# Performance work log

Hardware: AMD Instinct MI355X
Metric: run time of the kernel (lower is better)

The kernel has to match this reference:

```python
import jax, jax.numpy as jnp
import numpy as np

B, S, E = 4, 2048, 1024

def setup_inputs() -> dict:
    key = jax.random.key(0)
    ks = jax.random.split(key, 4)
    scale = 1.0 / np.sqrt(E)
    x = jax.random.normal(ks[0], (B, S, E), dtype=jnp.float32)
    Wq = jax.random.normal(ks[1], (E, E), dtype=jnp.float32) * scale
    Wk = jax.random.normal(ks[2], (E, E), dtype=jnp.float32) * scale
    Wv = jax.random.normal(ks[3], (E, E), dtype=jnp.float32) * scale
    bq = jnp.zeros((E,), dtype=jnp.float32)
    bk = jnp.zeros((E,), dtype=jnp.float32)
    bv = jnp.zeros((E,), dtype=jnp.float32)
    # causal mask: 1 where attention allowed, 0 where blocked (masked_fill(mask==0, -inf))
    mask = jnp.tril(jnp.ones((S, S), dtype=jnp.int32))
    return {"x": x, "mask": mask, "Wq": Wq, "bq": bq, "Wk": Wk, "bk": bk, "Wv": Wv, "bv": bv}

def reference(x, mask, Wq, bq, Wk, bk, Wv, bv):
    # x: (B, S, E); mask: (S, S) int, 0 -> -inf. Matches torch nn.Linear: x @ W.T + b
    Q = jnp.einsum('bse,fe->bsf', x, Wq) + bq
    K = jnp.einsum('bse,fe->bsf', x, Wk) + bk
    V = jnp.einsum('bse,fe->bsf', x, Wv) + bv
    inv_sqrt_e = 1.0 / jnp.sqrt(jnp.asarray(x.shape[-1], dtype=x.dtype))
    scores = jnp.einsum('bqe,bke->bqk', Q, K) * inv_sqrt_e  # (B, S, S)
    scores = jnp.where(mask[None, :, :] == 0, jnp.asarray(-jnp.inf, scores.dtype), scores)
    attn = jax.nn.softmax(scores, axis=-1)
    out = jnp.einsum('bqk,bke->bqe', attn, V)  # (B, S, E)
    return out
```

## Files before the change

kernel.cpp:

```cpp
#include <hip/hip_runtime.h>

#define B_ 4
#define S_ 2048
#define E_ 1024

typedef __attribute__((ext_vector_type(8))) short short8;
typedef __attribute__((ext_vector_type(4))) float f32x4;

__device__ __forceinline__ unsigned short f2bu(float f) {
  unsigned u = __builtin_bit_cast(unsigned, f);
  u = (u + 0x7FFFu + ((u >> 16) & 1u)) >> 16;
  return (unsigned short)u;
}

__device__ __forceinline__ void gload_lds16(const void* g, void* l) {
  __builtin_amdgcn_global_load_lds(
      (const __attribute__((address_space(1))) void*)g,
      (__attribute__((address_space(3))) void*)l, 16, 0, 0);
}

__global__ __launch_bounds__(256) void cvt_f32_bf16(
    const float* __restrict__ in, unsigned short* __restrict__ out, int n) {
  int i = blockIdx.x * 256 + threadIdx.x;
  if (i * 4 >= n) return;
  float4 v = ((const float4*)in)[i];
  ushort4 o;
  o.x = f2bu(v.x); o.y = f2bu(v.y); o.z = f2bu(v.z); o.w = f2bu(v.w);
  ((ushort4*)out)[i] = o;
}

__global__ __launch_bounds__(256) void cvt_w3(
    const float* __restrict__ w0, const float* __restrict__ w1,
    const float* __restrict__ w2, unsigned short* __restrict__ out, int n) {
  int z = blockIdx.z;
  const float* in = (z == 0) ? w0 : (z == 1) ? w1 : w2;
  int i = blockIdx.x * 256 + threadIdx.x;
  if (i * 4 >= n) return;
  float4 v = ((const float4*)in)[i];
  ushort4 o;
  o.x = f2bu(v.x); o.y = f2bu(v.y); o.z = f2bu(v.z); o.w = f2bu(v.w);
  ((ushort4*)(out + (long)z * n))[i] = o;
}

__global__ __launch_bounds__(256) void zden(float* __restrict__ d) {
  ((float4*)d)[blockIdx.x * 256 + threadIdx.x] = float4{0.f, 0.f, 0.f, 0.f};
}

template<int MODE>
__device__ __forceinline__ void gemm_body(
    const unsigned short* __restrict__ A, long sAz, int lda,
    const unsigned short* __restrict__ B, long sBz, int ldb,
    const float* __restrict__ bias0, const float* __restrict__ bias1,
    const float* __restrict__ bias2,
    void* __restrict__ C0, void* __restrict__ C1, void* __restrict__ C2,
    long sCz, int ldc, int K, float scale, float* __restrict__ denom,
    unsigned short* lA, unsigned short* lB, int bm, int bn, int bz) {
  constexpr int BK = 64;
  const unsigned short* Ab = A + (long)bz * sAz + (long)bm * 128 * lda;
  const unsigned short* Bb = B + (long)bz * sBz + (long)bn * 128 * ldb;
  int Keff = (MODE == 2) ? min(K, (bm + 1) * 128) : K;

  int tid = threadIdx.x;
  int l = tid & 63, w = tid >> 6;
  int wm = w >> 1, wn = w & 1;

  int srow = l >> 3;
  int schunk = (l & 7) * 8;
  const unsigned short* ga[4];
  const unsigned short* gb[4];
  unsigned short* lad[4];
  unsigned short* lbd[4];
#pragma unroll
  for (int i = 0; i < 4; i++) {
    int seg = i * 4 + w;
    int row = seg * 8 + srow;
    ga[i] = Ab + (long)row * lda + schunk;
    gb[i] = Bb + (long)row * ldb + schunk;
    lad[i] = &lA[seg * 512];
    lbd[i] = &lB[seg * 512];
  }
  int aoff[4], boff[4];
#pragma unroll
  for (int i = 0; i < 4; i++) {
    aoff[i] = (wm * 64 + i * 16 + (l & 15)) * BK + (l >> 4) * 8;
    boff[i] = (wn * 64 + i * 16 + (l & 15)) * BK + (l >> 4) * 8;
  }

  f32x4 acc[4][4] = {};

  for (int k0 = 0; k0 < Keff; k0 += BK) {
    __syncthreads();
#pragma unroll
    for (int i = 0; i < 4; i++) {
      gload_lds16(ga[i], lad[i]);
      gload_lds16(gb[i], lbd[i]);
    }
#pragma unroll
    for (int i = 0; i < 4; i++) { ga[i] += BK; gb[i] += BK; }
    __syncthreads();
#pragma unroll
    for (int kk = 0; kk < 2; kk++) {
      short8 af[4], bf[4];
#pragma unroll
      for (int i = 0; i < 4; i++) af[i] = *(const short8*)&lA[aoff[i] + kk * 32];
#pragma unroll
      for (int j = 0; j < 4; j++) bf[j] = *(const short8*)&lB[boff[j] + kk * 32];
#pragma unroll
      for (int i = 0; i < 4; i++)
#pragma unroll
        for (int j = 0; j < 4; j++)
          acc[i][j] = __builtin_amdgcn_mfma_f32_16x16x32_bf16(af[i], bf[j], acc[i][j], 0, 0, 0);
    }
  }

  int rh = l >> 4, cl = l & 15;
  long rowbase = (long)bm * 128 + wm * 64 + rh * 4;
  int colbase = bn * 128 + wn * 64 + cl;

  if constexpr (MODE == 0) {
    int seg = bn >> 3;
    const float* bias = (seg == 0) ? bias0 : (seg == 1) ? bias1 : bias2;
#pragma unroll
    for (int j = 0; j < 4; j++) {
      int c = colbase + j * 16;
      int cl_ = c & 1023;
      float bv_ = bias[cl_];
#pragma unroll
      for (int i = 0; i < 4; i++) {
        long r0 = rowbase + i * 16;
        f32x4 v = acc[i][j];
        if (seg < 2) {
          unsigned short* Ch = (unsigned short*)((seg == 0) ? C0 : C1);
#pragma unroll
          for (int t = 0; t < 4; t++)
            Ch[(r0 + t) * (long)E_ + cl_] = f2bu(v[t] + bv_);
        } else {
          unsigned short* Vt = (unsigned short*)C2;
          ushort4 pk;
          pk.x = f2bu(v[0] + bv_);
          pk.y = f2bu(v[1] + bv_);
          pk.z = f2bu(v[2] + bv_);
          pk.w = f2bu(v[3] + bv_);
          *(ushort4*)(Vt + (long)cl_ * (B_ * S_) + r0) = pk;
        }
      }
    }
  } else if constexpr (MODE == 1) {
    unsigned short* Ph = (unsigned short*)C0 + (long)bz * sCz;
    float rs[4][4] = {};
#pragma unroll
    for (int i = 0; i < 4; i++) {
      int r0 = (int)rowbase + i * 16;
#pragma unroll
      for (int t = 0; t < 4; t++) {
        int r = r0 + t;
#pragma unroll
        for (int j = 0; j < 4; j++) {
          int c = colbase + j * 16;
          float p = (c <= r) ? __expf(acc[i][j][t] * scale) : 0.f;
          Ph[(long)r * ldc + c] = f2bu(p);
          rs[i][t] += p;
        }
      }
    }
#pragma unroll
    for (int i = 0; i < 4; i++)
#pragma unroll
      for (int t = 0; t < 4; t++) {
        float s = rs[i][t];
        s += __shfl_xor(s, 1);
        s += __shfl_xor(s, 2);
        s += __shfl_xor(s, 4);
        s += __shfl_xor(s, 8);
        rs[i][t] = s;
      }
    if ((l & 15) == 0) {
      float* dz = denom + (long)bz * S_;
#pragma unroll
      for (int i = 0; i < 4; i++)
#pragma unroll
        for (int t = 0; t < 4; t++)
          atomicAdd(&dz[(int)rowbase + i * 16 + t], rs[i][t]);
    }
  } else {
    float* Cf = (float*)C0 + (long)bz * sCz;
    const float* dz = denom + (long)bz * S_;
    float rdn[4][4];
#pragma unroll
    for (int i = 0; i < 4; i++)
#pragma unroll
      for (int t = 0; t < 4; t++)
        rdn[i][t] = 1.0f / dz[(int)rowbase + i * 16 + t];
#pragma unroll
    for (int j = 0; j < 4; j++) {
      int c = colbase + j * 16;
#pragma unroll
      for (int i = 0; i < 4; i++) {
        long r0 = rowbase + i * 16;
        f32x4 v = acc[i][j];
#pragma unroll
        for (int t = 0; t < 4; t++)
          Cf[(r0 + t) * (long)ldc + c] = v[t] * rdn[i][t];
      }
    }
  }
}

__global__ __launch_bounds__(256, 3) void k_qkv(
    const unsigned short* __restrict__ A, const unsigned short* __restrict__ W,
    const float* __restrict__ bq, const float* __restrict__ bk,
    const float* __restrict__ bv,
    unsigned short* __restrict__ Qo, unsigned short* __restrict__ Ko,
    unsigned short* __restrict__ Vt) {
  __shared__ unsigned short lA[128 * 64];
  __shared__ unsigned short lB[128 * 64];
  int bid = blockIdx.y * 24 + blockIdx.x;
  int nb = (bid & 7) * 192 + (bid >> 3);
  gemm_body<0>(A, 0, E_, W, 0, E_, bq, bk, bv, Qo, Ko, Vt,
               0, E_, E_, 1.f, nullptr, lA, lB, nb / 24, nb % 24, 0);
}

__global__ __launch_bounds__(256, 3) void k_scores(
    const unsigned short* __restrict__ Q, const unsigned short* __restrict__ K,
    unsigned short* __restrict__ P, float* __restrict__ denom) {
  __shared__ unsigned short lA[128 * 64];
  __shared__ unsigned short lB[128 * 64];
  int t0 = blockIdx.x;
  int t = (t0 & 7) * 17 + (t0 >> 3);
  int bm = (int)((sqrtf(8.f * t + 1.f) - 1.f) * 0.5f);
  while ((bm + 1) * (bm + 2) / 2 <= t) bm++;
  while (bm * (bm + 1) / 2 > t) bm--;
  int bn = t - bm * (bm + 1) / 2;
  gemm_body<1>(Q, (long)S_ * E_, E_, K, (long)S_ * E_, E_,
               nullptr, nullptr, nullptr, P, nullptr, nullptr,
               (long)S_ * S_, S_, E_, 0.03125f, denom,
               lA, lB, bm, bn, blockIdx.z);
}

__global__ __launch_bounds__(256, 3) void k_pv(
    const unsigned short* __restrict__ P, const unsigned short* __restrict__ Vt,
    float* __restrict__ out, const float* __restrict__ denom) {
  __shared__ unsigned short lA[128 * 64];
  __shared__ unsigned short lB[128 * 64];
  int bm = 15 - blockIdx.y;
  gemm_body<2>(P, (long)S_ * S_, S_, Vt, (long)S_, B_ * S_,
               nullptr, nullptr, nullptr, out, nullptr, nullptr,
               (long)S_ * E_, E_, S_, 1.f, (float*)denom,
               lA, lB, bm, blockIdx.x, blockIdx.z);
}

extern "C" void kernel_launch(void* const* d_in, const int* in_sizes, int n_in,
                              void* d_out, int out_size, void* d_ws, size_t ws_size,
                              hipStream_t stream) {
  const float* x  = (const float*)d_in[0];
  const float* Wq = (const float*)d_in[2];
  const float* bq = (const float*)d_in[3];
  const float* Wk = (const float*)d_in[4];
  const float* bk = (const float*)d_in[5];
  const float* Wv = (const float*)d_in[6];
  const float* bv = (const float*)d_in[7];
  float* out = (float*)d_out;

  const long NX = (long)B_ * S_ * E_;
  const long NW = (long)E_ * E_;
  unsigned short* xb  = (unsigned short*)d_ws;
  unsigned short* wqb = xb + NX;
  unsigned short* Qb  = wqb + 3 * NW;
  unsigned short* Kb  = Qb + NX;
  unsigned short* Vtb = Kb + NX;
  unsigned short* Pb  = Vtb + NX;
  float* denom = (float*)(Pb + (long)B_ * S_ * S_);

  cvt_f32_bf16<<<8192, 256, 0, stream>>>(x, xb, (int)NX);
  cvt_w3<<<dim3(1024, 1, 3), 256, 0, stream>>>(Wq, Wk, Wv, wqb, (int)NW);
  zden<<<8, 256, 0, stream>>>(denom);

  k_qkv<<<dim3(24, 64), 256, 0, stream>>>(xb, wqb, bq, bk, bv, Qb, Kb, Vtb);

  k_scores<<<dim3(136, 1, 4), 256, 0, stream>>>(Qb, Kb, Pb, denom);

  k_pv<<<dim3(8, 16, 4), 256, 0, stream>>>(Pb, Vtb, out, denom);
}
```

Baseline: 165.3 us.

## Fuse x fp32-to-bf16 conversion into QKV GEMM A-tile loading

Removes the separate kernel that converted x to bf16. The QKV projection kernel now reads fp32 x directly into registers, converts it to bf16 in-kernel and writes it into LDS, prefetching the next K-slice during the MFMA loop. This saves one launch plus a full write and re-read of the bf16 copy of x. In exchange, each x tile is read in fp32 (twice the bytes) and converted 24 times, once per output column block, and the VGPR staging adds register pressure.

```diff
diff --git a/kernel.cpp b/kernel.cpp
--- a/kernel.cpp
+++ b/kernel.cpp
@@ -17,16 +17,6 @@
   __builtin_amdgcn_global_load_lds(
       (const __attribute__((address_space(1))) void*)g,
       (__attribute__((address_space(3))) void*)l, 16, 0, 0);
-}
-
-__global__ __launch_bounds__(256) void cvt_f32_bf16(
-    const float* __restrict__ in, unsigned short* __restrict__ out, int n) {
-  int i = blockIdx.x * 256 + threadIdx.x;
-  if (i * 4 >= n) return;
-  float4 v = ((const float4*)in)[i];
-  ushort4 o;
-  o.x = f2bu(v.x); o.y = f2bu(v.y); o.z = f2bu(v.z); o.w = f2bu(v.w);
-  ((ushort4*)out)[i] = o;
 }
 
 __global__ __launch_bounds__(256) void cvt_w3(
@@ -46,168 +36,8 @@
   ((float4*)d)[blockIdx.x * 256 + threadIdx.x] = float4{0.f, 0.f, 0.f, 0.f};
 }
 
-template<int MODE>
-__device__ __forceinline__ void gemm_body(
-    const unsigned short* __restrict__ A, long sAz, int lda,
-    const unsigned short* __restrict__ B, long sBz, int ldb,
-    const float* __restrict__ bias0, const float* __restrict__ bias1,
-    const float* __restrict__ bias2,
-    void* __restrict__ C0, void* __restrict__ C1, void* __restrict__ C2,
-    long sCz, int ldc, int K, float scale, float* __restrict__ denom,
-    unsigned short* lA, unsigned short* lB, int bm, int bn, int bz) {
-  constexpr int BK = 64;
-  const unsigned short* Ab = A + (long)bz * sAz + (long)bm * 128 * lda;
-  const unsigned short* Bb = B + (long)bz * sBz + (long)bn * 128 * ldb;
-  int Keff = (MODE == 2) ? min(K, (bm + 1) * 128) : K;
-
-  int tid = threadIdx.x;
-  int l = tid & 63, w = tid >> 6;
-  int wm = w >> 1, wn = w & 1;
-
-  int srow = l >> 3;
-  int schunk = (l & 7) * 8;
-  const unsigned short* ga[4];
-  const unsigned short* gb[4];
-  unsigned short* lad[4];
-  unsigned short* lbd[4];
-#pragma unroll
-  for (int i = 0; i < 4; i++) {
-    int seg = i * 4 + w;
-    int row = seg * 8 + srow;
-    ga[i] = Ab + (long)row * lda + schunk;
-    gb[i] = Bb + (long)row * ldb + schunk;
-    lad[i] = &lA[seg * 512];
-    lbd[i] = &lB[seg * 512];
-  }
-  int aoff[4], boff[4];
-#pragma unroll
-  for (int i = 0; i < 4; i++) {
-    aoff[i] = (wm * 64 + i * 16 + (l & 15)) * BK + (l >> 4) * 8;
-    boff[i] = (wn * 64 + i * 16 + (l & 15)) * BK + (l >> 4) * 8;
-  }
-
-  f32x4 acc[4][4] = {};
-
-  for (int k0 = 0; k0 < Keff; k0 += BK) {
-    __syncthreads();
-#pragma unroll
-    for (int i = 0; i < 4; i++) {
-      gload_lds16(ga[i], lad[i]);
-      gload_lds16(gb[i], lbd[i]);
-    }
-#pragma unroll
-    for (int i = 0; i < 4; i++) { ga[i] += BK; gb[i] += BK; }
-    __syncthreads();
-#pragma unroll
-    for (int kk = 0; kk < 2; kk++) {
-      short8 af[4], bf[4];
-#pragma unroll
-      for (int i = 0; i < 4; i++) af[i] = *(const short8*)&lA[aoff[i] + kk * 32];
-#pragma unroll
-      for (int j = 0; j < 4; j++) bf[j] = *(const short8*)&lB[boff[j] + kk * 32];
-#pragma unroll
-      for (int i = 0; i < 4; i++)
-#pragma unroll
-        for (int j = 0; j < 4; j++)
-          acc[i][j] = __builtin_amdgcn_mfma_f32_16x16x32_bf16(af[i], bf[j], acc[i][j], 0, 0, 0);
-    }
-  }
-
-  int rh = l >> 4, cl = l & 15;
-  long rowbase = (long)bm * 128 + wm * 64 + rh * 4;
-  int colbase = bn * 128 + wn * 64 + cl;
-
-  if constexpr (MODE == 0) {
-    int seg = bn >> 3;
-    const float* bias = (seg == 0) ? bias0 : (seg == 1) ? bias1 : bias2;
-#pragma unroll
-    for (int j = 0; j < 4; j++) {
-      int c = colbase + j * 16;
-      int cl_ = c & 1023;
-      float bv_ = bias[cl_];
-#pragma unroll
-      for (int i = 0; i < 4; i++) {
-        long r0 = rowbase + i * 16;
-        f32x4 v = acc[i][j];
-        if (seg < 2) {
-          unsigned short* Ch = (unsigned short*)((seg == 0) ? C0 : C1);
-#pragma unroll
-          for (int t = 0; t < 4; t++)
-            Ch[(r0 + t) * (long)E_ + cl_] = f2bu(v[t] + bv_);
-        } else {
-          unsigned short* Vt = (unsigned short*)C2;
-          ushort4 pk;
-          pk.x = f2bu(v[0] + bv_);
-          pk.y = f2bu(v[1] + bv_);
-          pk.z = f2bu(v[2] + bv_);
-          pk.w = f2bu(v[3] + bv_);
-          *(ushort4*)(Vt + (long)cl_ * (B_ * S_) + r0) = pk;
-        }
-      }
-    }
-  } else if constexpr (MODE == 1) {
-    unsigned short* Ph = (unsigned short*)C0 + (long)bz * sCz;
-    float rs[4][4] = {};
-#pragma unroll
-    for (int i = 0; i < 4; i++) {
-      int r0 = (int)rowbase + i * 16;
-#pragma unroll
-      for (int t = 0; t < 4; t++) {
-        int r = r0 + t;
-#pragma unroll
-        for (int j = 0; j < 4; j++) {
-          int c = colbase + j * 16;
-          float p = (c <= r) ? __expf(acc[i][j][t] * scale) : 0.f;
-          Ph[(long)r * ldc + c] = f2bu(p);
-          rs[i][t] += p;
-        }
-      }
-    }
-#pragma unroll
-    for (int i = 0; i < 4; i++)
-#pragma unroll
-      for (int t = 0; t < 4; t++) {
-        float s = rs[i][t];
-        s += __shfl_xor(s, 1);
-        s += __shfl_xor(s, 2);
-        s += __shfl_xor(s, 4);
-        s += __shfl_xor(s, 8);
-        rs[i][t] = s;
-      }
-    if ((l & 15) == 0) {
-      float* dz = denom + (long)bz * S_;
-#pragma unroll
-      for (int i = 0; i < 4; i++)
-#pragma unroll
-        for (int t = 0; t < 4; t++)
-          atomicAdd(&dz[(int)rowbase + i * 16 + t], rs[i][t]);
-    }
-  } else {
-    float* Cf = (float*)C0 + (long)bz * sCz;
-    const float* dz = denom + (long)bz * S_;
-    float rdn[4][4];
-#pragma unroll
-    for (int i = 0; i < 4; i++)
-#pragma unroll
-      for (int t = 0; t < 4; t++)
-        rdn[i][t] = 1.0f / dz[(int)rowbase + i * 16 + t];
-#pragma unroll
-    for (int j = 0; j < 4; j++) {
-      int c = colbase + j * 16;
-#pragma unroll
-      for (int i = 0; i < 4; i++) {
-        long r0 = rowbase + i * 16;
-        f32x4 v = acc[i][j];
-#pragma unroll
-        for (int t = 0; t < 4; t++)
-          Cf[(r0 + t) * (long)ldc + c] = v[t] * rdn[i][t];
-      }
-    }
-  }
-}
-
 __global__ __launch_bounds__(256, 3) void k_qkv(
-    const unsigned short* __restrict__ A, const unsigned short* __restrict__ W,
+    const float* __restrict__ X, const unsigned short* __restrict__ W,
     const float* __restrict__ bq, const float* __restrict__ bk,
     const float* __restrict__ bv,
     unsigned short* __restrict__ Qo, unsigned short* __restrict__ Ko,
@@ -216,8 +46,242 @@
   __shared__ unsigned short lB[128 * 64];
   int bid = blockIdx.y * 24 + blockIdx.x;
   int nb = (bid & 7) * 192 + (bid >> 3);
-  gemm_body<0>(A, 0, E_, W, 0, E_, bq, bk, bv, Qo, Ko, Vt,
-               0, E_, E_, 1.f, nullptr, lA, lB, nb / 24, nb % 24, 0);
+  int bm = nb / 24, bn = nb % 24;
+
+  int tid = threadIdx.x;
+  int l = tid & 63, w = tid >> 6;
+  int wm = w >> 1, wn = w & 1;
+
+  const unsigned short* Bb = W + (long)bn * 128 * E_;
+  int srow = l >> 3, schunk = (l & 7) * 8;
+  const unsigned short* gb[4];
+  unsigned short* lbd[4];
+#pragma unroll
+  for (int i = 0; i < 4; i++) {
+    int seg = i * 4 + w;
+    gb[i] = Bb + (long)(seg * 8 + srow) * E_ + schunk;
+    lbd[i] = &lB[seg * 512];
+  }
+
+  const float* Xb = X + (long)bm * 128 * E_ + (l & 7) * 8;
+  int arw = w * 8 + (l >> 3);
+  int awoff = w * 512 + l * 8;
+  float4 st[4][2];
+
+  int aoff[4], boff[4];
+#pragma unroll
+  for (int i = 0; i < 4; i++) {
+    aoff[i] = (wm * 64 + i * 16 + (l & 15)) * 64 + (l >> 4) * 8;
+    boff[i] = (wn * 64 + i * 16 + (l & 15)) * 64 + (l >> 4) * 8;
+  }
+
+#pragma unroll
+  for (int j = 0; j < 4; j++) {
+    const float* p = Xb + (long)(j * 32 + arw) * E_;
+    st[j][0] = *(const float4*)p;
+    st[j][1] = *(const float4*)(p + 4);
+  }
+
+  f32x4 acc[4][4] = {};
+
+  for (int k0 = 0; k0 < E_; k0 += 64) {
+    __syncthreads();
+#pragma unroll
+    for (int j = 0; j < 4; j++) {
+      short8 pk;
+      pk[0] = (short)f2bu(st[j][0].x); pk[1] = (short)f2bu(st[j][0].y);
+      pk[2] = (short)f2bu(st[j][0].z); pk[3] = (short)f2bu(st[j][0].w);
+      pk[4] = (short)f2bu(st[j][1].x); pk[5] = (short)f2bu(st[j][1].y);
+      pk[6] = (short)f2bu(st[j][1].z); pk[7] = (short)f2bu(st[j][1].w);
+      *(short8*)&lA[j * 2048 + awoff] = pk;
+    }
+#pragma unroll
+    for (int i = 0; i < 4; i++) { gload_lds16(gb[i], lbd[i]); gb[i] += 64; }
+    __syncthreads();
+
+    if (k0 + 64 < E_) {
+#pragma unroll
+      for (int j = 0; j < 4; j++) {
+        const float* p = Xb + (long)(j * 32 + arw) * E_ + (k0 + 64);
+        st[j][0] = *(const float4*)p;
+        st[j][1] = *(const float4*)(p + 4);
+      }
+    }
+
+#pragma unroll
+    for (int kk = 0; kk < 2; kk++) {
+      short8 af[4], bf[4];
+#pragma unroll
+      for (int i = 0; i < 4; i++) af[i] = *(const short8*)&lA[aoff[i] + kk * 32];
+#pragma unroll
+      for (int j = 0; j < 4; j++) bf[j] = *(const short8*)&lB[boff[j] + kk * 32];
+#pragma unroll
+      for (int i = 0; i < 4; i++)
+#pragma unroll
+        for (int j = 0; j < 4; j++)
+          acc[i][j] = __builtin_amdgcn_mfma_f32_16x16x32_bf16(af[i], bf[j], acc[i][j], 0, 0, 0);
+    }
+  }
+
+  int rh = l >> 4, cl = l & 15;
+  long rowbase = (long)bm * 128 + wm * 64 + rh * 4;
+  int colbase = bn * 128 + wn * 64 + cl;
+  int seg = bn >> 3;
+  const float* bias = (seg == 0) ? bq : (seg == 1) ? bk : bv;
+#pragma unroll
+  for (int j = 0; j < 4; j++) {
+    int c = colbase + j * 16;
+    int cl_ = c & 1023;
+    float bv_ = bias[cl_];
+#pragma unroll
+    for (int i = 0; i < 4; i++) {
+      long r0 = rowbase + i * 16;
+      f32x4 v = acc[i][j];
+      if (seg < 2) {
+        unsigned short* Ch = (seg == 0) ? Qo : Ko;
+#pragma unroll
+        for (int t = 0; t < 4; t++)
+          Ch[(r0 + t) * (long)E_ + cl_] = f2bu(v[t] + bv_);
+      } else {
+        ushort4 pk;
+        pk.x = f2bu(v[0] + bv_);
+        pk.y = f2bu(v[1] + bv_);
+        pk.z = f2bu(v[2] + bv_);
+        pk.w = f2bu(v[3] + bv_);
+        *(ushort4*)(Vt + (long)cl_ * (B_ * S_) + r0) = pk;
+      }
+    }
+  }
+}
+
+template<int MODE>
+__device__ __forceinline__ void gemm_body(
+    const unsigned short* __restrict__ A, long sAz, int lda,
+    const unsigned short* __restrict__ B, long sBz, int ldb,
+    void* __restrict__ C0, long sCz, int ldc, int K, float scale,
+    float* __restrict__ denom,
+    unsigned short* lA, unsigned short* lB, int bm, int bn, int bz) {
+  constexpr int BK = 64;
+  const unsigned short* Ab = A + (long)bz * sAz + (long)bm * 128 * lda;
+  const unsigned short* Bb = B + (long)bz * sBz + (long)bn * 128 * ldb;
+  int Keff = (MODE == 2) ? min(K, (bm + 1) * 128) : K;
+
+  int tid = threadIdx.x;
+  int l = tid & 63, w = tid >> 6;
+  int wm = w >> 1, wn = w & 1;
+
+  int srow = l >> 3;
+  int schunk = (l & 7) * 8;
+  const unsigned short* ga[4];
+  const unsigned short* gb[4];
+  unsigned short* lad[4];
+  unsigned short* lbd[4];
+#pragma unroll
+  for (int i = 0; i < 4; i++) {
+    int seg = i * 4 + w;
+    int row = seg * 8 + srow;
+    ga[i] = Ab + (long)row * lda + schunk;
+    gb[i] = Bb + (long)row * ldb + schunk;
+    lad[i] = &lA[seg * 512];
+    lbd[i] = &lB[seg * 512];
+  }
+  int aoff[4], boff[4];
+#pragma unroll
+  for (int i = 0; i < 4; i++) {
+    aoff[i] = (wm * 64 + i * 16 + (l & 15)) * BK + (l >> 4) * 8;
+    boff[i] = (wn * 64 + i * 16 + (l & 15)) * BK + (l >> 4) * 8;
+  }
+
+  f32x4 acc[4][4] = {};
+
+  for (int k0 = 0; k0 < Keff; k0 += BK) {
+    __syncthreads();
+#pragma unroll
+    for (int i = 0; i < 4; i++) {
+      gload_lds16(ga[i], lad[i]);
+      gload_lds16(gb[i], lbd[i]);
+    }
+#pragma unroll
+    for (int i = 0; i < 4; i++) { ga[i] += BK; gb[i] += BK; }
+    __syncthreads();
+#pragma unroll
+    for (int kk = 0; kk < 2; kk++) {
+      short8 af[4], bf[4];
+#pragma unroll
+      for (int i = 0; i < 4; i++) af[i] = *(const short8*)&lA[aoff[i] + kk * 32];
+#pragma unroll
+      for (int j = 0; j < 4; j++) bf[j] = *(const short8*)&lB[boff[j] + kk * 32];
+#pragma unroll
+      for (int i = 0; i < 4; i++)
+#pragma unroll
+        for (int j = 0; j < 4; j++)
+          acc[i][j] = __builtin_amdgcn_mfma_f32_16x16x32_bf16(af[i], bf[j], acc[i][j], 0, 0, 0);
+    }
+  }
+
+  int rh = l >> 4, cl = l & 15;
+  long rowbase = (long)bm * 128 + wm * 64 + rh * 4;
+  int colbase = bn * 128 + wn * 64 + cl;
+
+  if constexpr (MODE == 1) {
+    unsigned short* Ph = (unsigned short*)C0 + (long)bz * sCz;
+    float rs[4][4] = {};
+#pragma unroll
+    for (int i = 0; i < 4; i++) {
+      int r0 = (int)rowbase + i * 16;
+#pragma unroll
+      for (int t = 0; t < 4; t++) {
+        int r = r0 + t;
+#pragma unroll
+        for (int j = 0; j < 4; j++) {
+          int c = colbase + j * 16;
+          float p = (c <= r) ? __expf(acc[i][j][t] * scale) : 0.f;
+          Ph[(long)r * ldc + c] = f2bu(p);
+          rs[i][t] += p;
+        }
+      }
+    }
+#pragma unroll
+    for (int i = 0; i < 4; i++)
+#pragma unroll
+      for (int t = 0; t < 4; t++) {
+        float s = rs[i][t];
+        s += __shfl_xor(s, 1);
+        s += __shfl_xor(s, 2);
+        s += __shfl_xor(s, 4);
+        s += __shfl_xor(s, 8);
+        rs[i][t] = s;
+      }
+    if ((l & 15) == 0) {
+      float* dz = denom + (long)bz * S_;
+#pragma unroll
+      for (int i = 0; i < 4; i++)
+#pragma unroll
+        for (int t = 0; t < 4; t++)
+          atomicAdd(&dz[(int)rowbase + i * 16 + t], rs[i][t]);
+    }
+  } else {
+    float* Cf = (float*)C0 + (long)bz * sCz;
+    const float* dz = denom + (long)bz * S_;
+    float rdn[4][4];
+#pragma unroll
+    for (int i = 0; i < 4; i++)
+#pragma unroll
+      for (int t = 0; t < 4; t++)
+        rdn[i][t] = 1.0f / dz[(int)rowbase + i * 16 + t];
+#pragma unroll
+    for (int j = 0; j < 4; j++) {
+      int c = colbase + j * 16;
+#pragma unroll
+      for (int i = 0; i < 4; i++) {
+        long r0 = rowbase + i * 16;
+        f32x4 v = acc[i][j];
+#pragma unroll
+        for (int t = 0; t < 4; t++)
+          Cf[(r0 + t) * (long)ldc + c] = v[t] * rdn[i][t];
+      }
+    }
+  }
 }
 
 __global__ __launch_bounds__(256, 3) void k_scores(
@@ -232,8 +296,7 @@
   while (bm * (bm + 1) / 2 > t) bm--;
   int bn = t - bm * (bm + 1) / 2;
   gemm_body<1>(Q, (long)S_ * E_, E_, K, (long)S_ * E_, E_,
-               nullptr, nullptr, nullptr, P, nullptr, nullptr,
-               (long)S_ * S_, S_, E_, 0.03125f, denom,
+               P, (long)S_ * S_, S_, E_, 0.03125f, denom,
                lA, lB, bm, bn, blockIdx.z);
 }
 
@@ -244,8 +307,7 @@
   __shared__ unsigned short lB[128 * 64];
   int bm = 15 - blockIdx.y;
   gemm_body<2>(P, (long)S_ * S_, S_, Vt, (long)S_, B_ * S_,
-               nullptr, nullptr, nullptr, out, nullptr, nullptr,
-               (long)S_ * E_, E_, S_, 1.f, (float*)denom,
+               out, (long)S_ * E_, E_, S_, 1.f, (float*)denom,
                lA, lB, bm, blockIdx.x, blockIdx.z);
 }
 
@@ -263,19 +325,17 @@
 
   const long NX = (long)B_ * S_ * E_;
   const long NW = (long)E_ * E_;
-  unsigned short* xb  = (unsigned short*)d_ws;
-  unsigned short* wqb = xb + NX;
+  unsigned short* wqb = (unsigned short*)d_ws;
   unsigned short* Qb  = wqb + 3 * NW;
   unsigned short* Kb  = Qb + NX;
   unsigned short* Vtb = Kb + NX;
   unsigned short* Pb  = Vtb + NX;
   float* denom = (float*)(Pb + (long)B_ * S_ * S_);
 
-  cvt_f32_bf16<<<8192, 256, 0, stream>>>(x, xb, (int)NX);
   cvt_w3<<<dim3(1024, 1, 3), 256, 0, stream>>>(Wq, Wk, Wv, wqb, (int)NW);
   zden<<<8, 256, 0, stream>>>(denom);
 
-  k_qkv<<<dim3(24, 64), 256, 0, stream>>>(xb, wqb, bq, bk, bv, Qb, Kb, Vtb);
+  k_qkv<<<dim3(24, 64), 256, 0, stream>>>(x, wqb, bq, bk, bv, Qb, Kb, Vtb);
 
   k_scores<<<dim3(136, 1, 4), 256, 0, stream>>>(Qb, Kb, Pb, denom);
 
```

Measured after the change: 170.6 us. 1.03x slower.
